# Performance work log

Measured on AMD Instinct MI355X. Metric: run time of the kernel, lower is better.

## Reference

```python
import jax, jax.numpy as jnp
import numpy as np

L, B = 64, 7          # n_layers, n_bit_options
EPS = 0.02            # sinkhorn entropic regularizer
ITERS = 200           # sinkhorn iterations
TINY = 1e-40


def setup_inputs() -> dict:
    key = jax.random.key(0)
    k1, k2, k3, k4 = jax.random.split(key, 4)
    theta = jax.random.normal(k1, (L, B), dtype=jnp.float32)
    phi = jax.random.normal(k2, (B,), dtype=jnp.float32)
    # layer sizes (param counts), positive; matches layer_sizes buffer usage
    n = jax.random.uniform(k3, (L,), dtype=jnp.float32, minval=4096.0, maxval=262144.0)
    sens = jax.random.uniform(k4, (L,), dtype=jnp.float32)
    sens = sens / sens.sum()  # update_sensitivity normalizes to a distribution
    bits = jnp.arange(2, 2 + B, dtype=jnp.float32)
    err = 2.0 ** (-2.0 * bits)  # quantization error per bitwidth
    return {"theta": theta, "phi": phi, "n": n, "sens": sens, "err": err}


def reference(theta, phi, n, sens, err):
    # DiffAllocator.compute_P
    a = n / n.sum()                         # row marginal (buffer 'a')
    b = jax.nn.softmax(phi)                 # col marginal b()
    C = (n * sens)[:, None] * err[None, :]  # build_cost: [L,B]
    K = -(C - theta) / EPS                  # log-kernel
    log_a = jnp.log(a + TINY)
    log_b = jnp.log(b + TINY)
    f0 = jnp.zeros((L,), dtype=theta.dtype)
    g0 = jnp.zeros((B,), dtype=theta.dtype)

    def step(carry, _):
        f, g = carry
        f = log_a - jax.scipy.special.logsumexp(K + g[None, :], axis=1)
        g = log_b - jax.scipy.special.logsumexp(K + f[:, None], axis=0)
        return (f, g), None

    (f, g), _ = jax.lax.scan(step, (f0, g0), None, length=ITERS)
    P = jnp.exp(K + f[:, None] + g[None, :])
    return P / (P.sum() + TINY)
```

## Files before the change

kernel.cpp:

```cpp
#include <hip/hip_runtime.h>
#include <math.h>

#define NB 7
#define EPS_ 0.02f
#define ITERS1_ 120
#define ITERS2_ 80
#define TINY_ 1e-40f
#define LOG2E_ 1.4426950408889634f
#define LN2_   0.6931471805599453f

__device__ __forceinline__ float exp2_hw(float x) {
#if __has_builtin(__builtin_amdgcn_exp2f)
    return __builtin_amdgcn_exp2f(x);
#else
    return __expf(x * LN2_);
#endif
}
__device__ __forceinline__ float log2_hw(float x) {
#if __has_builtin(__builtin_amdgcn_logf)
    return __builtin_amdgcn_logf(x);
#else
    return __logf(x) * LOG2E_;
#endif
}
__device__ __forceinline__ float rcp_hw(float x) {
#if __has_builtin(__builtin_amdgcn_rcpf)
    return __builtin_amdgcn_rcpf(x);
#else
    return 1.0f / x;
#endif
}

template <int CTRL>
__device__ __forceinline__ float dpp_ident(float identity, float x) {
    return __int_as_float(__builtin_amdgcn_update_dpp(
        __float_as_int(identity), __float_as_int(x), CTRL, 0xF, 0xF, false));
}
__device__ __forceinline__ float readlane63(float x) {
    return __int_as_float(__builtin_amdgcn_readlane(__float_as_int(x), 63));
}
__device__ __forceinline__ float wave_sum_bcast(float s) {
    s += dpp_ident<0x111>(0.f, s);
    s += dpp_ident<0x112>(0.f, s);
    s += dpp_ident<0x114>(0.f, s);
    s += dpp_ident<0x118>(0.f, s);
    s += dpp_ident<0x142>(0.f, s);
    s += dpp_ident<0x143>(0.f, s);
    return readlane63(s);
}
__device__ __forceinline__ float wave_max_bcast(float m) {
    const float NI = __int_as_float(0xff800000);
    m = fmaxf(m, dpp_ident<0x111>(NI, m));
    m = fmaxf(m, dpp_ident<0x112>(NI, m));
    m = fmaxf(m, dpp_ident<0x114>(NI, m));
    m = fmaxf(m, dpp_ident<0x118>(NI, m));
    m = fmaxf(m, dpp_ident<0x142>(NI, m));
    m = fmaxf(m, dpp_ident<0x143>(NI, m));
    return readlane63(m);
}

#define STRIDE_ 9

__global__ __launch_bounds__(448) void sinkhorn_kernel(
    const float* __restrict__ theta,
    const float* __restrict__ phi,
    const float* __restrict__ n,
    const float* __restrict__ sens,
    const float* __restrict__ err,
    float* __restrict__ out)
{
    const int tid  = threadIdx.x;
    const int lane = tid & 63;
    const int wid  = tid >> 6;

    __shared__ float bufEA[2][64 * STRIDE_ + 8];
    __shared__ float bufAA[2][64 * STRIDE_ + 8];
    __shared__ float ldsS[8];

    const float ni = n[lane];
    const float si = sens[lane];
    const float ej = err[wid];
    const float th = theta[lane * NB + wid];

    const float nsum   = wave_sum_bcast(ni);
    const float aT     = ni / nsum + TINY_;
    const float log_a2 = log2_hw(aT);

    float t2v0 = phi[0] * LOG2E_, t2v1 = phi[1] * LOG2E_,
          t2v2 = phi[2] * LOG2E_, t2v3 = phi[3] * LOG2E_,
          t2v4 = phi[4] * LOG2E_, t2v5 = phi[5] * LOG2E_,
          t2v6 = phi[6] * LOG2E_;
    float pmax = t2v0;
    pmax = fmaxf(pmax, t2v1); pmax = fmaxf(pmax, t2v2);
    pmax = fmaxf(pmax, t2v3); pmax = fmaxf(pmax, t2v4);
    pmax = fmaxf(pmax, t2v5); pmax = fmaxf(pmax, t2v6);
    float psum = exp2_hw(t2v0 - pmax);
    psum += exp2_hw(t2v1 - pmax); psum += exp2_hw(t2v2 - pmax);
    psum += exp2_hw(t2v3 - pmax); psum += exp2_hw(t2v4 - pmax);
    psum += exp2_hw(t2v5 - pmax); psum += exp2_hw(t2v6 - pmax);
    const float lps  = log2_hw(psum);
    const float myt2 = phi[wid] * LOG2E_;
    const float bTj  = exp2_hw(myt2 - pmax - lps) + TINY_;
    const float lb2j = log2_hw(bTj);
    const float cbj  = lb2j - log_a2;

    const float kscale = LOG2E_ / EPS_;
    float t = (th - ni * si * ej) * kscale - lb2j;

    const float LOF = __int_as_float(0x0D800000);
    const float HIF = __int_as_float(0x71800000);
    const int   base = lane * STRIDE_ + wid;
    const int   rb   = lane * STRIDE_;

    for (int it = 0; it < ITERS1_; ++it) {
        const int p = it & 1;
        const float a = t + cbj;
        bufEA[p][base] = exp2_hw(a);
        bufAA[p][base] = a;
        __syncthreads();

        const float e0 = bufEA[p][rb + 0], e1 = bufEA[p][rb + 1],
                    e2 = bufEA[p][rb + 2], e3 = bufEA[p][rb + 3],
                    e4 = bufEA[p][rb + 4], e5 = bufEA[p][rb + 5],
                    e6 = bufEA[p][rb + 6];
        const float s = ((e0 + e1) + (e2 + e3)) + ((e4 + e5) + e6);
        float L;
        const bool ok = (s >= LOF) && (s <= HIF);
        if (__ballot(ok) == ~0ull) {
            L = log2_hw(s);
        } else {
            const float a0 = bufAA[p][rb + 0], a1 = bufAA[p][rb + 1],
                        a2 = bufAA[p][rb + 2], a3 = bufAA[p][rb + 3],
                        a4 = bufAA[p][rb + 4], a5 = bufAA[p][rb + 5],
                        a6 = bufAA[p][rb + 6];
            const float m = fmaxf(fmaxf(fmaxf(a0, a1), fmaxf(a2, a3)),
                                  fmaxf(fmaxf(a4, a5), a6));
            const float s2 = ((exp2_hw(a0 - m) + exp2_hw(a1 - m))
                            + (exp2_hw(a2 - m) + exp2_hw(a3 - m)))
                           + ((exp2_hw(a4 - m) + exp2_hw(a5 - m))
                            + exp2_hw(a6 - m));
            L = m + log2_hw(s2);
        }

        const float q = t - L;
        const float e = exp2_hw(q);
        const float ss = wave_sum_bcast(e);
        if (ss >= LOF && ss <= HIF) {
            t = q - log2_hw(ss);
        } else {
            const float M   = wave_max_bcast(q);
            const float e2  = exp2_hw(q - M);
            const float ss2 = wave_sum_bcast(e2);
            t = q - (M + log2_hw(ss2));
        }
    }

    float U = exp2_hw(t);
    const float Bj = exp2_hw(cbj);

    for (int it2 = 0; it2 < ITERS2_; ++it2) {
        const int p = it2 & 1;
        bufEA[p][base] = U * Bj;
        __syncthreads();
        const float p0 = bufEA[p][rb + 0], p1 = bufEA[p][rb + 1],
                    p2 = bufEA[p][rb + 2], p3 = bufEA[p][rb + 3],
                    p4 = bufEA[p][rb + 4], p5 = bufEA[p][rb + 5],
                    p6 = bufEA[p][rb + 6];
        const float s  = ((p0 + p1) + (p2 + p3)) + ((p4 + p5) + p6);
        const float rs = rcp_hw(s);
        const float w  = U * rs;
        const float ss = wave_sum_bcast(w);
        U = w * rcp_hw(ss);
    }

    const float pr = U * bTj;
    const float cs = wave_sum_bcast(pr);
    if (lane == 0) ldsS[wid] = cs;
    __syncthreads();
    const float total = ((ldsS[0] + ldsS[1]) + (ldsS[2] + ldsS[3]))
                      + ((ldsS[4] + ldsS[5]) + ldsS[6]);
    out[lane * NB + wid] = pr * (1.0f / (total + TINY_));
}

extern "C" void kernel_launch(void* const* d_in, const int* in_sizes, int n_in,
                              void* d_out, int out_size, void* d_ws, size_t ws_size,
                              hipStream_t stream) {
    const float* theta = (const float*)d_in[0];
    const float* phi   = (const float*)d_in[1];
    const float* n     = (const float*)d_in[2];
    const float* sens  = (const float*)d_in[3];
    const float* err   = (const float*)d_in[4];
    float* out = (float*)d_out;

    sinkhorn_kernel<<<1, 448, 0, stream>>>(theta, phi, n, sens, err, out);
}
```

Measured before the change: 111.3 us.

## Replace log-domain sinkhorn phase with mantissa/exponent split representation

The first Sinkhorn phase now stores each kernel entry as a mantissa plus an integer exponent instead of a log value. Row normalisation uses integer max and ldexp alignment instead of exp2/log2. Column normalisation uses reciprocals with a lazily updated shared exponent offset, so the per-iteration transcendental exp/log calls and the branchy log-sum-exp fallback go away. The risk is extra integer and ldexp work, wider float2 LDS traffic, and possible precision or range loss in the exponent bookkeeping.

```diff
diff --git a/kernel.cpp b/kernel.cpp
--- a/kernel.cpp
+++ b/kernel.cpp
@@ -30,11 +30,36 @@
     return 1.0f / x;
 #endif
 }
+__device__ __forceinline__ float ldexp_hw(float x, int e) {
+#if __has_builtin(__builtin_amdgcn_ldexpf)
+    return __builtin_amdgcn_ldexpf(x, e);
+#else
+    float r; asm("v_ldexp_f32 %0, %1, %2" : "=v"(r) : "v"(x), "v"(e)); return r;
+#endif
+}
+__device__ __forceinline__ float frexp_mant_hw(float x) {
+#if __has_builtin(__builtin_amdgcn_frexp_mantf)
+    return __builtin_amdgcn_frexp_mantf(x);
+#else
+    float r; asm("v_frexp_mant_f32 %0, %1" : "=v"(r) : "v"(x)); return r;
+#endif
+}
+__device__ __forceinline__ int frexp_exp_hw(float x) {
+#if __has_builtin(__builtin_amdgcn_frexp_expf)
+    return __builtin_amdgcn_frexp_expf(x);
+#else
+    int r; asm("v_frexp_exp_i32_f32 %0, %1" : "=v"(r) : "v"(x)); return r;
+#endif
+}
 
 template <int CTRL>
 __device__ __forceinline__ float dpp_ident(float identity, float x) {
     return __int_as_float(__builtin_amdgcn_update_dpp(
         __float_as_int(identity), __float_as_int(x), CTRL, 0xF, 0xF, false));
+}
+template <int CTRL>
+__device__ __forceinline__ int dpp_ident_i(int identity, int x) {
+    return __builtin_amdgcn_update_dpp(identity, x, CTRL, 0xF, 0xF, false);
 }
 __device__ __forceinline__ float readlane63(float x) {
     return __int_as_float(__builtin_amdgcn_readlane(__float_as_int(x), 63));
@@ -48,18 +73,18 @@
     s += dpp_ident<0x143>(0.f, s);
     return readlane63(s);
 }
-__device__ __forceinline__ float wave_max_bcast(float m) {
-    const float NI = __int_as_float(0xff800000);
-    m = fmaxf(m, dpp_ident<0x111>(NI, m));
-    m = fmaxf(m, dpp_ident<0x112>(NI, m));
-    m = fmaxf(m, dpp_ident<0x114>(NI, m));
-    m = fmaxf(m, dpp_ident<0x118>(NI, m));
-    m = fmaxf(m, dpp_ident<0x142>(NI, m));
-    m = fmaxf(m, dpp_ident<0x143>(NI, m));
-    return readlane63(m);
-}
-
-#define STRIDE_ 9
+__device__ __forceinline__ int wave_maxi_bcast(int m) {
+    const int NI = (int)0x80000000;
+    m = max(m, dpp_ident_i<0x111>(NI, m));
+    m = max(m, dpp_ident_i<0x112>(NI, m));
+    m = max(m, dpp_ident_i<0x114>(NI, m));
+    m = max(m, dpp_ident_i<0x118>(NI, m));
+    m = max(m, dpp_ident_i<0x142>(NI, m));
+    m = max(m, dpp_ident_i<0x143>(NI, m));
+    return __builtin_amdgcn_readlane(m, 63);
+}
+
+#define RS_ 9
 
 __global__ __launch_bounds__(448) void sinkhorn_kernel(
     const float* __restrict__ theta,
@@ -73,9 +98,8 @@
     const int lane = tid & 63;
     const int wid  = tid >> 6;
 
-    __shared__ float bufEA[2][64 * STRIDE_ + 8];
-    __shared__ float bufAA[2][64 * STRIDE_ + 8];
-    __shared__ float ldsS[8];
+    __shared__ float2 buf[2][64 * RS_ + 4];
+    __shared__ float  ldsS[8];
 
     const float ni = n[lane];
     const float si = sens[lane];
@@ -103,73 +127,78 @@
     const float bTj  = exp2_hw(myt2 - pmax - lps) + TINY_;
     const float lb2j = log2_hw(bTj);
     const float cbj  = lb2j - log_a2;
+    const float b2c  = exp2_hw(cbj);
+    const float ibc  = exp2_hw(-cbj);
 
     const float kscale = LOG2E_ / EPS_;
-    float t = (th - ni * si * ej) * kscale - lb2j;
-
-    const float LOF = __int_as_float(0x0D800000);
-    const float HIF = __int_as_float(0x71800000);
-    const int   base = lane * STRIDE_ + wid;
-    const int   rb   = lane * STRIDE_;
+    const float y  = (th - ni * si * ej) * kscale - log_a2;
+    const float yi = rintf(y);
+    int   F = (int)yi;
+    float v = exp2_hw(y - yi);
+
+    int XcS = 0;
+    const float LO80f = __int_as_float(0x17800000);
+    const float HI80f = __int_as_float(0x67800000);
+
+    const int base = lane * RS_ + wid;
+    const int rb   = lane * RS_;
 
     for (int it = 0; it < ITERS1_; ++it) {
         const int p = it & 1;
-        const float a = t + cbj;
-        bufEA[p][base] = exp2_hw(a);
-        bufAA[p][base] = a;
+        buf[p][base] = make_float2(v, __int_as_float(F));
         __syncthreads();
 
-        const float e0 = bufEA[p][rb + 0], e1 = bufEA[p][rb + 1],
-                    e2 = bufEA[p][rb + 2], e3 = bufEA[p][rb + 3],
-                    e4 = bufEA[p][rb + 4], e5 = bufEA[p][rb + 5],
-                    e6 = bufEA[p][rb + 6];
-        const float s = ((e0 + e1) + (e2 + e3)) + ((e4 + e5) + e6);
-        float L;
-        const bool ok = (s >= LOF) && (s <= HIF);
-        if (__ballot(ok) == ~0ull) {
-            L = log2_hw(s);
-        } else {
-            const float a0 = bufAA[p][rb + 0], a1 = bufAA[p][rb + 1],
-                        a2 = bufAA[p][rb + 2], a3 = bufAA[p][rb + 3],
-                        a4 = bufAA[p][rb + 4], a5 = bufAA[p][rb + 5],
-                        a6 = bufAA[p][rb + 6];
-            const float m = fmaxf(fmaxf(fmaxf(a0, a1), fmaxf(a2, a3)),
-                                  fmaxf(fmaxf(a4, a5), a6));
-            const float s2 = ((exp2_hw(a0 - m) + exp2_hw(a1 - m))
-                            + (exp2_hw(a2 - m) + exp2_hw(a3 - m)))
-                           + ((exp2_hw(a4 - m) + exp2_hw(a5 - m))
-                            + exp2_hw(a6 - m));
-            L = m + log2_hw(s2);
+        const float2 c0 = buf[p][rb + 0], c1 = buf[p][rb + 1],
+                     c2 = buf[p][rb + 2], c3 = buf[p][rb + 3],
+                     c4 = buf[p][rb + 4], c5 = buf[p][rb + 5],
+                     c6 = buf[p][rb + 6];
+        const int F0 = __float_as_int(c0.y), F1 = __float_as_int(c1.y),
+                  F2 = __float_as_int(c2.y), F3 = __float_as_int(c3.y),
+                  F4 = __float_as_int(c4.y), F5 = __float_as_int(c5.y),
+                  F6 = __float_as_int(c6.y);
+        const int X = max(max(max(F0, F1), max(F2, F3)),
+                          max(max(F4, F5), F6));
+        const float f0 = ldexp_hw(c0.x, F0 - X), f1 = ldexp_hw(c1.x, F1 - X),
+                    f2 = ldexp_hw(c2.x, F2 - X), f3 = ldexp_hw(c3.x, F3 - X),
+                    f4 = ldexp_hw(c4.x, F4 - X), f5 = ldexp_hw(c5.x, F5 - X),
+                    f6 = ldexp_hw(c6.x, F6 - X);
+        const float s  = ((f0 + f1) + (f2 + f3)) + ((f4 + f5) + f6);
+        const float rs = rcp_hw(s);
+
+        const float w  = (v * ibc) * rs;
+        const int   Fw = F - X;
+
+        int d = Fw - XcS;
+        float h  = ldexp_hw(w, d);
+        float ss = wave_sum_bcast(h);
+        if (!(ss >= LO80f && ss <= HI80f)) {
+            const int M = wave_maxi_bcast(Fw);
+            d  = Fw - M;
+            h  = ldexp_hw(w, d);
+            ss = wave_sum_bcast(h);
+            XcS = M;
         }
 
-        const float q = t - L;
-        const float e = exp2_hw(q);
-        const float ss = wave_sum_bcast(e);
-        if (ss >= LOF && ss <= HIF) {
-            t = q - log2_hw(ss);
-        } else {
-            const float M   = wave_max_bcast(q);
-            const float e2  = exp2_hw(q - M);
-            const float ss2 = wave_sum_bcast(e2);
-            t = q - (M + log2_hw(ss2));
-        }
+        const float z = (w * rcp_hw(ss)) * b2c;
+        v = frexp_mant_hw(z);
+        F = frexp_exp_hw(z) + d;
     }
 
-    float U = exp2_hw(t);
-    const float Bj = exp2_hw(cbj);
+    float U = ldexp_hw(v * ibc, F);
+    const float Bj = b2c;
 
     for (int it2 = 0; it2 < ITERS2_; ++it2) {
         const int p = it2 & 1;
-        bufEA[p][base] = U * Bj;
+        buf[p][base].x = U * Bj;
         __syncthreads();
-        const float p0 = bufEA[p][rb + 0], p1 = bufEA[p][rb + 1],
-                    p2 = bufEA[p][rb + 2], p3 = bufEA[p][rb + 3],
-                    p4 = bufEA[p][rb + 4], p5 = bufEA[p][rb + 5],
-                    p6 = bufEA[p][rb + 6];
+        const float p0 = buf[p][rb + 0].x, p1 = buf[p][rb + 1].x,
+                    p2 = buf[p][rb + 2].x, p3 = buf[p][rb + 3].x,
+                    p4 = buf[p][rb + 4].x, p5 = buf[p][rb + 5].x,
+                    p6 = buf[p][rb + 6].x;
         const float s  = ((p0 + p1) + (p2 + p3)) + ((p4 + p5) + p6);
-        const float rs = rcp_hw(s);
-        const float w  = U * rs;
-        const float ss = wave_sum_bcast(w);
+        const float rsv = rcp_hw(s);
+        const float w   = U * rsv;
+        const float ss  = wave_sum_bcast(w);
         U = w * rcp_hw(ss);
     }
 
```

New measurement: 120.0 us. +7.8%, slower.
